# Kernel optimization log

Hardware: AMD Instinct MI355X
Metric: run time of the kernel (lower is better)

Reference implementation:

```python
import jax, jax.numpy as jnp
import numpy as np

SEQ, DIM = 65536, 1024

def setup_inputs() -> dict:
    key = jax.random.key(0)
    k1, k2, k3, k4, k5 = jax.random.split(key, 5)
    # xavier_uniform gain=1.414 bound for (dim,dim): gain*sqrt(6/(dim+dim))
    bound = 1.414 * np.sqrt(6.0 / (DIM + DIM))
    qbound = 1.414 * np.sqrt(6.0 / (1 + DIM))
    return {
        "v": jax.random.normal(k1, (SEQ, DIM), dtype=jnp.float32),
        "W1": jax.random.uniform(k2, (DIM, DIM), jnp.float32, -bound, bound),
        "W2": jax.random.uniform(k3, (DIM, DIM), jnp.float32, -bound, bound),
        "q": jax.random.uniform(k4, (1, DIM), jnp.float32, -qbound, qbound),
        "b": jax.random.normal(k5, (1,), dtype=jnp.float32) * 0.02,  # nn.Linear(dim,1).bias, shape [1]
    }

def reference(v, W1, W2, q, b):
    # vn = last timestep; per-step math: q @ (W1 @ v_i + W2 @ vn + b)
    vn = v[-1]                                     # [dim]
    ctx = W2 @ vn + b                              # [dim] (b is [1], broadcasts)
    inp = jnp.einsum('dk,sk->sd', W1, v) + ctx     # [seq, dim]
    scores = inp @ q[0]                            # [seq]  (q is [1,dim])
    # output = scores^T @ v, then squeeze -> [dim]
    return scores @ v
```

## Files before the change

### kernel.cpp

```cpp
#include <hip/hip_runtime.h>

#define SEQ 65536
#define DIM 1024


__global__ void k_init(float* __restrict__ ws, float* __restrict__ out) {
    int t = blockIdx.x * 256 + threadIdx.x;
    if (t < 4096) ws[t] = 0.0f;
    if (t < DIM)  out[t] = 0.0f;
}

__global__ void k_qmat(const float* __restrict__ W1,
                       const float* __restrict__ W2,
                       const float* __restrict__ q,
                       float* __restrict__ ws) {
    const float* M = (blockIdx.z == 0) ? W1 : W2;
    float* dst = ws + blockIdx.z * DIM;
    int col = blockIdx.x * 256 + threadIdx.x;
    int d0  = blockIdx.y * 128;
    float s = 0.0f;
#pragma unroll 8
    for (int d = 0; d < 128; ++d) {
        s += q[d0 + d] * M[(size_t)(d0 + d) * DIM + col];
    }
    atomicAdd(&dst[col], s);
}

__global__ void k_c0(const float* __restrict__ v,
                     const float* __restrict__ q,
                     const float* __restrict__ b,
                     float* __restrict__ ws) {
    __shared__ float red[1024];
    int t = threadIdx.x;
    const float* vn = v + (size_t)(SEQ - 1) * DIM;
    float val = ws[1024 + t] * vn[t] + b[0] * q[t];
    red[t] = val;
    __syncthreads();
    for (int off = 512; off > 0; off >>= 1) {
        if (t < off) red[t] += red[t + off];
        __syncthreads();
    }
    if (t == 0) ws[2048] = red[0];
}

__launch_bounds__(256, 4)
__global__ void k_main(const float* __restrict__ v,
                       const float* __restrict__ ws,
                       float* __restrict__ part, int nb) {
    __shared__ float sacc[DIM];
    const int tid  = threadIdx.x;
    const int lane = tid & 63;
    const int wid  = tid >> 6;

    const float c0 = ws[2048];
    const float4* wq = (const float4*)(ws + lane * 16);
    float4 w0 = wq[0], w1 = wq[1], w2 = wq[2], w3 = wq[3];

    float4 a0 = {0,0,0,0}, a1 = {0,0,0,0}, a2 = {0,0,0,0}, a3 = {0,0,0,0};

    const int gw = blockIdx.x * 4 + wid;
    const int nw = nb * 4;

    for (int s = gw; s < SEQ; s += nw) {
        const float4* row = (const float4*)(v + (size_t)s * DIM + lane * 16);
        float4 ra = row[0], rb = row[1], rc = row[2], rd = row[3];

        float p = ra.x * w0.x + ra.y * w0.y + ra.z * w0.z + ra.w * w0.w
                + rb.x * w1.x + rb.y * w1.y + rb.z * w1.z + rb.w * w1.w
                + rc.x * w2.x + rc.y * w2.y + rc.z * w2.z + rc.w * w2.w
                + rd.x * w3.x + rd.y * w3.y + rd.z * w3.z + rd.w * w3.w;
#pragma unroll
        for (int off = 1; off < 64; off <<= 1)
            p += __shfl_xor(p, off, 64);
        float score = p + c0;

        a0.x += score * ra.x; a0.y += score * ra.y; a0.z += score * ra.z; a0.w += score * ra.w;
        a1.x += score * rb.x; a1.y += score * rb.y; a1.z += score * rb.z; a1.w += score * rb.w;
        a2.x += score * rc.x; a2.y += score * rc.y; a2.z += score * rc.z; a2.w += score * rc.w;
        a3.x += score * rd.x; a3.y += score * rd.y; a3.z += score * rd.z; a3.w += score * rd.w;
    }

    for (int i = tid; i < DIM; i += 256) sacc[i] = 0.0f;
    __syncthreads();

    for (int wv = 0; wv < 4; ++wv) {
        if (wid == wv) {
            float* s0 = sacc + lane * 16;
            s0[0]  += a0.x; s0[1]  += a0.y; s0[2]  += a0.z; s0[3]  += a0.w;
            s0[4]  += a1.x; s0[5]  += a1.y; s0[6]  += a1.z; s0[7]  += a1.w;
            s0[8]  += a2.x; s0[9]  += a2.y; s0[10] += a2.z; s0[11] += a2.w;
            s0[12] += a3.x; s0[13] += a3.y; s0[14] += a3.z; s0[15] += a3.w;
        }
        __syncthreads();
    }

    float* dst = part + (size_t)blockIdx.x * DIM;
    for (int i = tid; i < DIM; i += 256) dst[i] = sacc[i];
}

__global__ void k_reduce(const float* __restrict__ part,
                         float* __restrict__ out, int nb) {
    int col = blockIdx.x * 256 + threadIdx.x;
    int chunk = (nb + 31) / 32;
    int b0 = blockIdx.y * chunk;
    int b1 = min(nb, b0 + chunk);
    float s = 0.0f;
    for (int bdx = b0; bdx < b1; ++bdx)
        s += part[(size_t)bdx * DIM + col];
    atomicAdd(&out[col], s);
}

extern "C" void kernel_launch(void* const* d_in, const int* in_sizes, int n_in,
                              void* d_out, int out_size, void* d_ws, size_t ws_size,
                              hipStream_t stream) {
    const float* v  = (const float*)d_in[0];
    const float* W1 = (const float*)d_in[1];
    const float* W2 = (const float*)d_in[2];
    const float* q  = (const float*)d_in[3];
    const float* b  = (const float*)d_in[4];
    float* out = (float*)d_out;
    float* ws  = (float*)d_ws;

    size_t avail = ws_size / sizeof(float);
    int nb = 1024;
    if ((size_t)(4096 + (size_t)nb * DIM) > avail)
        nb = (int)((avail - 4096) / DIM);
    if (nb < 1) nb = 1;
    float* part = ws + 4096;

    k_init<<<dim3(16), dim3(256), 0, stream>>>(ws, out);
    k_qmat<<<dim3(4, 8, 2), dim3(256), 0, stream>>>(W1, W2, q, ws);
    k_c0<<<dim3(1), dim3(1024), 0, stream>>>(v, q, b, ws);
    k_main<<<dim3(nb), dim3(256), 0, stream>>>(v, ws, part, nb);
    k_reduce<<<dim3(4, 32), dim3(256), 0, stream>>>(part, out, nb);
}
```

Baseline: 390.2 us.

## Unroll main loop two rows per wave, drop init/reduce kernels, use atomics

The main streaming loop now processes two rows per wave per iteration with nontemporal loads, which doubles the memory requests in flight. The separate init and reduce kernels are removed. Partial sums of q·W are written to workspace slots and summed in a prep kernel, which also zeroes the output. Each block atomically adds its shared accumulator into the output, trading a second pass over partials for contended atomics across 1024 blocks. The workspace size check is dropped and the block count is fixed.

```diff
diff --git a/kernel.cpp b/kernel.cpp
--- a/kernel.cpp
+++ b/kernel.cpp
@@ -2,82 +2,106 @@
 
 #define SEQ 65536
 #define DIM 1024
+#define NB  1024
+#define NW  (NB * 4)
 
+typedef float f32x4 __attribute__((ext_vector_type(4)));
 
-__global__ void k_init(float* __restrict__ ws, float* __restrict__ out) {
-    int t = blockIdx.x * 256 + threadIdx.x;
-    if (t < 4096) ws[t] = 0.0f;
-    if (t < DIM)  out[t] = 0.0f;
-}
 
 __global__ void k_qmat(const float* __restrict__ W1,
                        const float* __restrict__ W2,
                        const float* __restrict__ q,
                        float* __restrict__ ws) {
-    const float* M = (blockIdx.z == 0) ? W1 : W2;
-    float* dst = ws + blockIdx.z * DIM;
+    const float* M = blockIdx.z ? W2 : W1;
     int col = blockIdx.x * 256 + threadIdx.x;
-    int d0  = blockIdx.y * 128;
+    int d0  = blockIdx.y * 64;
     float s = 0.0f;
 #pragma unroll 8
-    for (int d = 0; d < 128; ++d) {
+    for (int d = 0; d < 64; ++d)
         s += q[d0 + d] * M[(size_t)(d0 + d) * DIM + col];
-    }
-    atomicAdd(&dst[col], s);
+    ws[3072 + (blockIdx.z * 16 + blockIdx.y) * DIM + col] = s;
 }
 
-__global__ void k_c0(const float* __restrict__ v,
-                     const float* __restrict__ q,
-                     const float* __restrict__ b,
-                     float* __restrict__ ws) {
+__global__ void k_prep(const float* __restrict__ v,
+                       const float* __restrict__ q,
+                       const float* __restrict__ b,
+                       float* __restrict__ ws,
+                       float* __restrict__ out) {
     __shared__ float red[1024];
     int t = threadIdx.x;
+    const float* p = ws + 3072;
+    float w = 0.0f, w2 = 0.0f;
+#pragma unroll
+    for (int y = 0; y < 16; ++y) {
+        w  += p[y * DIM + t];
+        w2 += p[(16 + y) * DIM + t];
+    }
+    ws[t] = w;
     const float* vn = v + (size_t)(SEQ - 1) * DIM;
-    float val = ws[1024 + t] * vn[t] + b[0] * q[t];
-    red[t] = val;
+    red[t] = w2 * vn[t] + b[0] * q[t];
     __syncthreads();
     for (int off = 512; off > 0; off >>= 1) {
         if (t < off) red[t] += red[t + off];
         __syncthreads();
     }
     if (t == 0) ws[2048] = red[0];
+    out[t] = 0.0f;
 }
 
 __launch_bounds__(256, 4)
 __global__ void k_main(const float* __restrict__ v,
                        const float* __restrict__ ws,
-                       float* __restrict__ part, int nb) {
+                       float* __restrict__ out) {
     __shared__ float sacc[DIM];
     const int tid  = threadIdx.x;
     const int lane = tid & 63;
     const int wid  = tid >> 6;
 
     const float c0 = ws[2048];
-    const float4* wq = (const float4*)(ws + lane * 16);
-    float4 w0 = wq[0], w1 = wq[1], w2 = wq[2], w3 = wq[3];
+    const f32x4* wq = (const f32x4*)(ws + lane * 16);
+    f32x4 w0 = wq[0], w1 = wq[1], w2 = wq[2], w3 = wq[3];
 
-    float4 a0 = {0,0,0,0}, a1 = {0,0,0,0}, a2 = {0,0,0,0}, a3 = {0,0,0,0};
+    f32x4 a0 = 0.0f, a1 = 0.0f, a2 = 0.0f, a3 = 0.0f;
 
     const int gw = blockIdx.x * 4 + wid;
-    const int nw = nb * 4;
 
-    for (int s = gw; s < SEQ; s += nw) {
-        const float4* row = (const float4*)(v + (size_t)s * DIM + lane * 16);
-        float4 ra = row[0], rb = row[1], rc = row[2], rd = row[3];
+    for (int s = gw; s < SEQ; s += 2 * NW) {
+        const int sB = s + NW;
+        const bool hb = sB < SEQ;
 
-        float p = ra.x * w0.x + ra.y * w0.y + ra.z * w0.z + ra.w * w0.w
-                + rb.x * w1.x + rb.y * w1.y + rb.z * w1.z + rb.w * w1.w
-                + rc.x * w2.x + rc.y * w2.y + rc.z * w2.z + rc.w * w2.w
-                + rd.x * w3.x + rd.y * w3.y + rd.z * w3.z + rd.w * w3.w;
+        const f32x4* rA = (const f32x4*)(v + (size_t)s * DIM + lane * 16);
+        f32x4 ra0 = __builtin_nontemporal_load(&rA[0]);
+        f32x4 ra1 = __builtin_nontemporal_load(&rA[1]);
+        f32x4 ra2 = __builtin_nontemporal_load(&rA[2]);
+        f32x4 ra3 = __builtin_nontemporal_load(&rA[3]);
+
+        const f32x4* rB = (const f32x4*)(v + (size_t)(hb ? sB : s) * DIM + lane * 16);
+        f32x4 rb0 = __builtin_nontemporal_load(&rB[0]);
+        f32x4 rb1 = __builtin_nontemporal_load(&rB[1]);
+        f32x4 rb2 = __builtin_nontemporal_load(&rB[2]);
+        f32x4 rb3 = __builtin_nontemporal_load(&rB[3]);
+
+        float pA = ra0.x*w0.x + ra0.y*w0.y + ra0.z*w0.z + ra0.w*w0.w
+                 + ra1.x*w1.x + ra1.y*w1.y + ra1.z*w1.z + ra1.w*w1.w
+                 + ra2.x*w2.x + ra2.y*w2.y + ra2.z*w2.z + ra2.w*w2.w
+                 + ra3.x*w3.x + ra3.y*w3.y + ra3.z*w3.z + ra3.w*w3.w;
+        float pB = rb0.x*w0.x + rb0.y*w0.y + rb0.z*w0.z + rb0.w*w0.w
+                 + rb1.x*w1.x + rb1.y*w1.y + rb1.z*w1.z + rb1.w*w1.w
+                 + rb2.x*w2.x + rb2.y*w2.y + rb2.z*w2.z + rb2.w*w2.w
+                 + rb3.x*w3.x + rb3.y*w3.y + rb3.z*w3.z + rb3.w*w3.w;
+
 #pragma unroll
-        for (int off = 1; off < 64; off <<= 1)
-            p += __shfl_xor(p, off, 64);
-        float score = p + c0;
+        for (int off = 1; off < 64; off <<= 1) {
+            pA += __shfl_xor(pA, off, 64);
+            pB += __shfl_xor(pB, off, 64);
+        }
+        float scoreA = pA + c0;
+        float scoreB = pB + c0;
 
-        a0.x += score * ra.x; a0.y += score * ra.y; a0.z += score * ra.z; a0.w += score * ra.w;
-        a1.x += score * rb.x; a1.y += score * rb.y; a1.z += score * rb.z; a1.w += score * rb.w;
-        a2.x += score * rc.x; a2.y += score * rc.y; a2.z += score * rc.z; a2.w += score * rc.w;
-        a3.x += score * rd.x; a3.y += score * rd.y; a3.z += score * rd.z; a3.w += score * rd.w;
+        a0 += scoreA * ra0; a1 += scoreA * ra1; a2 += scoreA * ra2; a3 += scoreA * ra3;
+        if (hb) {
+            a0 += scoreB * rb0; a1 += scoreB * rb1; a2 += scoreB * rb2; a3 += scoreB * rb3;
+        }
     }
 
     for (int i = tid; i < DIM; i += 256) sacc[i] = 0.0f;
@@ -94,20 +118,8 @@
         __syncthreads();
     }
 
-    float* dst = part + (size_t)blockIdx.x * DIM;
-    for (int i = tid; i < DIM; i += 256) dst[i] = sacc[i];
-}
-
-__global__ void k_reduce(const float* __restrict__ part,
-                         float* __restrict__ out, int nb) {
-    int col = blockIdx.x * 256 + threadIdx.x;
-    int chunk = (nb + 31) / 32;
-    int b0 = blockIdx.y * chunk;
-    int b1 = min(nb, b0 + chunk);
-    float s = 0.0f;
-    for (int bdx = b0; bdx < b1; ++bdx)
-        s += part[(size_t)bdx * DIM + col];
-    atomicAdd(&out[col], s);
+    for (int i = tid; i < DIM; i += 256)
+        atomicAdd(&out[i], sacc[i]);
 }
 
 extern "C" void kernel_launch(void* const* d_in, const int* in_sizes, int n_in,
@@ -121,16 +133,7 @@
     float* out = (float*)d_out;
     float* ws  = (float*)d_ws;
 
-    size_t avail = ws_size / sizeof(float);
-    int nb = 1024;
-    if ((size_t)(4096 + (size_t)nb * DIM) > avail)
-        nb = (int)((avail - 4096) / DIM);
-    if (nb < 1) nb = 1;
-    float* part = ws + 4096;
-
-    k_init<<<dim3(16), dim3(256), 0, stream>>>(ws, out);
-    k_qmat<<<dim3(4, 8, 2), dim3(256), 0, stream>>>(W1, W2, q, ws);
-    k_c0<<<dim3(1), dim3(1024), 0, stream>>>(v, q, b, ws);
-    k_main<<<dim3(nb), dim3(256), 0, stream>>>(v, ws, part, nb);
-    k_reduce<<<dim3(4, 32), dim3(256), 0, stream>>>(part, out, nb);
+    k_qmat<<<dim3(4, 16, 2), dim3(256), 0, stream>>>(W1, W2, q, ws);
+    k_prep<<<dim3(1), dim3(1024), 0, stream>>>(v, q, b, ws, out);
+    k_main<<<dim3(NB), dim3(256), 0, stream>>>(v, ws, out);
 }
```

New measurement: 380.8 us. -2.4%, faster.
